# Kernel tuning notes

Measured on AMD Instinct MI355X. Metric: run time of the kernel, lower is better.

Reference implementation:

```python
import jax, jax.numpy as jnp
import numpy as np

LN_EPS = 1e-5


def _layernorm(x, gamma, beta):
    mu = jnp.mean(x, axis=-1, keepdims=True)
    var = jnp.mean(jnp.square(x - mu), axis=-1, keepdims=True)
    return (x - mu) / jnp.sqrt(var + LN_EPS) * gamma + beta


def setup_inputs() -> dict:
    key = jax.random.key(0)
    ks = jax.random.split(key, 4)
    B, T, H, L = 32, 2048, 512, 2
    scale = 1.0 / np.sqrt(H)  # matches torch GRU uniform(-1/sqrt(H),1/sqrt(H)) scale
    x = jax.random.normal(ks[0], (B, T, H), dtype=jnp.float32)
    W_ih = jax.random.normal(ks[1], (L, 3 * H, H), dtype=jnp.float32) * scale
    W_hh = jax.random.normal(ks[2], (L, 3 * H, H), dtype=jnp.float32) * scale
    b_ih = jnp.zeros((L, 3 * H), dtype=jnp.float32)
    b_hh = jnp.zeros((L, 3 * H), dtype=jnp.float32)
    gamma = jnp.ones((H,), dtype=jnp.float32)
    beta = jnp.zeros((H,), dtype=jnp.float32)
    return {"x": x, "gamma": gamma, "beta": beta,
            "W_ih": W_ih, "W_hh": W_hh, "b_ih": b_ih, "b_hh": b_hh}


def reference(x, gamma, beta, W_ih, W_hh, b_ih, b_hh):
    # LayerNorm then multi-layer GRU (PyTorch gate order: r, z, n).
    B, T, H = x.shape
    L = W_ih.shape[0]
    h = _layernorm(x, gamma, beta)
    for l in range(L):
        # Precompute input projections for all timesteps: [B, T, 3H]
        xp = jnp.einsum('bth,gh->btg', h, W_ih[l]) + b_ih[l]
        Whh_l = W_hh[l]
        bhh_l = b_hh[l]

        def step(h_prev, xp_t):
            hp = h_prev @ Whh_l.T + bhh_l              # [B, 3H]
            xr, xz, xn = jnp.split(xp_t, 3, axis=-1)
            hr, hz, hn = jnp.split(hp, 3, axis=-1)
            r = jax.nn.sigmoid(xr + hr)
            z = jax.nn.sigmoid(xz + hz)
            n = jnp.tanh(xn + r * hn)
            h_new = (1.0 - z) * n + z * h_prev
            return h_new, h_new

        h0 = jnp.zeros((B, H), dtype=x.dtype)
        _, ys = jax.lax.scan(step, h0, jnp.swapaxes(xp, 0, 1))  # [T, B, H]
        h = jnp.swapaxes(ys, 0, 1)
    return h
```

## Files before the change

### kernel.cpp

```cpp
#include <hip/hip_runtime.h>
#include <hip/hip_fp16.h>

typedef float f32x4 __attribute__((ext_vector_type(4)));
typedef float f32x16 __attribute__((ext_vector_type(16)));
typedef _Float16 half8 __attribute__((ext_vector_type(8)));
typedef _Float16 half2t __attribute__((ext_vector_type(2)));
typedef unsigned int u32;
typedef u32 u32x4v __attribute__((ext_vector_type(4)));

#define DEVI static __device__ __forceinline__

constexpr int BATCH = 32;
constexpr int TLEN  = 2048;
constexpr int HDIM  = 512;
constexpr int G3    = 1536;

DEVI float fast_sigmoid(float x) { return 1.0f / (1.0f + __expf(-x)); }

DEVI float fast_tanh(float x) {
  const float ax = fabsf(x);
  const float t = __expf(-2.0f * ax);
  const float r = (1.0f - t) / (1.0f + t);
  return copysignf(r, x);
}

DEVI u32 pack2h(float a, float b) {
  return __builtin_bit_cast(u32, __builtin_amdgcn_cvt_pkrtz(a, b));
}

DEVI u32 llc_load32(const u32* p) {
  return __hip_atomic_load(p, __ATOMIC_RELAXED, __HIP_MEMORY_SCOPE_AGENT);
}
DEVI void llc_store32(u32* p, u32 v) {
  __hip_atomic_store(p, v, __ATOMIC_RELAXED, __HIP_MEMORY_SCOPE_AGENT);
}

DEVI u32x4v llc_load128_async(const u32* p) {
  u32x4v r;
  asm volatile("global_load_dwordx4 %0, %1, off sc0 sc1" : "=&v"(r) : "v"(p));
  return r;
}

__global__ void convert_weights(const float* __restrict__ wih, const float* __restrict__ whh,
                                _Float16* __restrict__ wih_h, _Float16* __restrict__ whh_h)
{
  const size_t n = (size_t)2 * G3 * HDIM;
  for (size_t i = (size_t)blockIdx.x * blockDim.x + threadIdx.x; i < n;
       i += (size_t)gridDim.x * blockDim.x) {
    wih_h[i] = (_Float16)wih[i];
    whh_h[i] = (_Float16)whh[i];
  }
}

__global__ __launch_bounds__(256) void ln_kernel(const float* __restrict__ x,
    const float* __restrict__ gamma, const float* __restrict__ beta,
    _Float16* __restrict__ out)
{
  const int row = blockIdx.x;
  const int tid = threadIdx.x;
  const float* xr = x + (size_t)row * HDIM;
  float a = xr[tid], b = xr[tid + 256];
  float s = a + b, ss = a * a + b * b;
#pragma unroll
  for (int m = 1; m < 64; m <<= 1) {
    s  += __shfl_xor(s, m, 64);
    ss += __shfl_xor(ss, m, 64);
  }
  __shared__ float sb[8];
  const int w = tid >> 6;
  if ((tid & 63) == 0) { sb[w] = s; sb[4 + w] = ss; }
  __syncthreads();
  s  = sb[0] + sb[1] + sb[2] + sb[3];
  ss = sb[4] + sb[5] + sb[6] + sb[7];
  const float mu   = s * (1.0f / HDIM);
  const float var  = ss * (1.0f / HDIM) - mu * mu;
  const float rstd = rsqrtf(var + 1e-5f);
  out[(size_t)row * HDIM + tid]       = (_Float16)((a - mu) * rstd * gamma[tid] + beta[tid]);
  out[(size_t)row * HDIM + tid + 256] = (_Float16)((b - mu) * rstd * gamma[tid + 256] + beta[tid + 256]);
}

__global__ __launch_bounds__(256) void gemm_f16(
    const _Float16* __restrict__ A, const _Float16* __restrict__ W,
    const float* __restrict__ bias, _Float16* __restrict__ C,
    int t0, int lgT)
{
  __shared__ _Float16 As[128][40];
  __shared__ _Float16 Bs[128][40];
  const int bm = blockIdx.x;
  const int bn = blockIdx.y;
  const int tid = threadIdx.x;
  const int lane = tid & 63;
  const int wv = tid >> 6;
  const int wm = wv >> 1, wn = wv & 1;
  const int l15 = lane & 15, g4 = lane >> 4;
  const int tmask = (1 << lgT) - 1;

  f32x4 zero4 = {0.f, 0.f, 0.f, 0.f};
  f32x4 acc[4][4];
#pragma unroll
  for (int i = 0; i < 4; ++i) {
#pragma unroll
    for (int j = 0; j < 4; ++j) acc[i][j] = zero4;
  }

  const int srow = tid >> 2;
  const int scol = (tid & 3) * 8;
  size_t arow[2];
#pragma unroll
  for (int r2 = 0; r2 < 2; ++r2) {
    int m = bm * 128 + r2 * 64 + srow;
    int b = m >> lgT, tt = m & tmask;
    arow[r2] = ((size_t)b * TLEN + (size_t)(t0 + tt)) * HDIM;
  }
  const size_t brow0 = (size_t)(bn * 128 + srow) * HDIM;

  for (int kt = 0; kt < HDIM; kt += 32) {
#pragma unroll
    for (int r2 = 0; r2 < 2; ++r2) {
      *(uint4*)&As[r2 * 64 + srow][scol] = *(const uint4*)&A[arow[r2] + kt + scol];
      *(uint4*)&Bs[r2 * 64 + srow][scol] = *(const uint4*)&W[brow0 + (size_t)r2 * 64 * HDIM + kt + scol];
    }
    __syncthreads();
    half8 af[4], bf[4];
#pragma unroll
    for (int i = 0; i < 4; ++i) af[i] = *(const half8*)&As[wm * 64 + i * 16 + l15][g4 * 8];
#pragma unroll
    for (int j = 0; j < 4; ++j) bf[j] = *(const half8*)&Bs[wn * 64 + j * 16 + l15][g4 * 8];
#pragma unroll
    for (int i = 0; i < 4; ++i) {
#pragma unroll
      for (int j = 0; j < 4; ++j)
        acc[i][j] = __builtin_amdgcn_mfma_f32_16x16x32_f16(af[i], bf[j], acc[i][j], 0, 0, 0);
    }
    __syncthreads();
  }
#pragma unroll
  for (int j = 0; j < 4; ++j) {
    const int col = bn * 128 + wn * 64 + j * 16 + l15;
    const float bi = bias[col];
#pragma unroll
    for (int i = 0; i < 4; ++i) {
      const int mrow = bm * 128 + wm * 64 + i * 16 + g4 * 4;
#pragma unroll
      for (int r = 0; r < 4; ++r)
        C[(size_t)(mrow + r) * G3 + col] = (_Float16)(acc[i][j][r] + bi);
    }
  }
}

__global__ void init_sync(u32* __restrict__ hbufs, u32* __restrict__ flags)
{
  const int i = blockIdx.x * 256 + threadIdx.x;
  if (i < 6 * 8192) hbufs[i] = 0u;
  if (i < 64) flags[i] = 0u;
}

__global__ __launch_bounds__(512, 1) void gru_fused(
    const u32* __restrict__ xp,
    const u32* __restrict__ whh,
    const u32* __restrict__ wih2,
    const float* __restrict__ bhh,
    const float* __restrict__ bih2,
    float* __restrict__ out,
    u32* __restrict__ h1buf,
    u32* __restrict__ h2buf,
    u32* __restrict__ flags,
    int t0, int t1, int lgT)
{
  const int l2 = blockIdx.x >> 4;
  const int c  = blockIdx.x & 15;
  const int tid = threadIdx.x;
  const int lane = tid & 63;
  const int w = tid >> 6;
  const int l31 = lane & 31;
  const int kh = lane >> 5;

  __shared__ __align__(16) u32 st_l[32 * 260];
  __shared__ __align__(16) u32 h1_l[32 * 260];
  __shared__ float sg_h[96 * 33];
  __shared__ float sg_i[96 * 33];

  half8 bf[32];
  const bool mfma_w = (w < 3) || (l2 && w < 6);
  if (mfma_w) {
    const int gt = (w < 3) ? w : w - 3;
    const int grow = gt * 512 + c * 32 + l31;
    const u32* wsrc = (w < 3) ? (whh + (size_t)l2 * (G3 * 256)) : wih2;
#pragma unroll
    for (int ks = 0; ks < 32; ++ks)
      bf[ks] = *(const half8*)&wsrc[(size_t)grow * 256 + ks * 8 + kh * 4];
  }

  const int dp = tid & 15;
  const int ga = tid >> 4;
  const float* bhh_l = bhh + l2 * G3;
  float biasH[3][2], biasI[3][2];
#pragma unroll
  for (int gt = 0; gt < 3; ++gt) {
    biasH[gt][0] = bhh_l[gt * 512 + c * 32 + 2 * dp];
    biasH[gt][1] = bhh_l[gt * 512 + c * 32 + 2 * dp + 1];
    biasI[gt][0] = l2 ? bih2[gt * 512 + c * 32 + 2 * dp] : 0.0f;
    biasI[gt][1] = l2 ? bih2[gt * 512 + c * 32 + 2 * dp + 1] : 0.0f;
  }

  for (int t = t0; t < t1; ++t) {
    u32 xu[3];
    if (!l2) {
      const size_t row = ((size_t)(ga << lgT) + (size_t)(t - t0)) * 768;
#pragma unroll
      for (int gt = 0; gt < 3; ++gt)
        xu[gt] = xp[row + gt * 256 + c * 16 + dp];
    }
    if (w == 0) {
      const int n1 = l2 ? (t + 1) : t;
      const int n2 = l2 ? t       : (t - 3);
      const int fl = lane & 15;
      while (true) {
        const int f1 = (int)llc_load32(&flags[fl]);
        const int f2 = (int)llc_load32(&flags[32 + fl]);
        if (__all((int)((f1 >= n1) && (f2 >= n2)))) break;
        __builtin_amdgcn_s_sleep(1);
      }
    }
    __syncthreads();

    const u32* stsrc = l2 ? (h2buf + (size_t)(t & 1) * 8192)
                          : (h1buf + (size_t)(t & 3) * 8192);
    u32x4v sv0, sv1, sv2, sv3, hv0, hv1, hv2, hv3;
    {
      const u32* sp = stsrc + (tid << 2);
      sv0 = llc_load128_async(sp);
      sv1 = llc_load128_async(sp + 2048);
      sv2 = llc_load128_async(sp + 4096);
      sv3 = llc_load128_async(sp + 6144);
      if (l2) {
        const u32* hp = h1buf + (size_t)((t + 1) & 3) * 8192 + (tid << 2);
        hv0 = llc_load128_async(hp);
        hv1 = llc_load128_async(hp + 2048);
        hv2 = llc_load128_async(hp + 4096);
        hv3 = llc_load128_async(hp + 6144);
      }
    }
    asm volatile("s_waitcnt vmcnt(0)" ::: "memory");
    __builtin_amdgcn_sched_barrier(0);
    {
      const int r0 = tid >> 6;
      const int cc = (tid << 2) & 255;
      *(u32x4v*)&st_l[(0  + r0) * 260 + cc] = sv0;
      *(u32x4v*)&st_l[(8  + r0) * 260 + cc] = sv1;
      *(u32x4v*)&st_l[(16 + r0) * 260 + cc] = sv2;
      *(u32x4v*)&st_l[(24 + r0) * 260 + cc] = sv3;
      if (l2) {
        *(u32x4v*)&h1_l[(0  + r0) * 260 + cc] = hv0;
        *(u32x4v*)&h1_l[(8  + r0) * 260 + cc] = hv1;
        *(u32x4v*)&h1_l[(16 + r0) * 260 + cc] = hv2;
        *(u32x4v*)&h1_l[(24 + r0) * 260 + cc] = hv3;
      }
    }
    __syncthreads();

    const u32 hpp = st_l[ga * 260 + c * 16 + dp];

    if (mfma_w) {
      f32x16 acc;
#pragma unroll
      for (int i = 0; i < 16; ++i) acc[i] = 0.0f;
      const u32* asrc = (w < 3) ? st_l : h1_l;
#pragma unroll
      for (int ks = 0; ks < 32; ++ks) {
        const half8 af = *(const half8*)&asrc[l31 * 260 + ks * 8 + kh * 4];
        acc = __builtin_amdgcn_mfma_f32_32x32x16_f16(af, bf[ks], acc, 0, 0, 0);
      }
      const int gt = (w < 3) ? w : w - 3;
      float* sg = (w < 3) ? sg_h : sg_i;
#pragma unroll
      for (int r = 0; r < 16; ++r) {
        const int grp = (r & 3) + 8 * (r >> 2) + 4 * kh;
        sg[(gt * 32 + l31) * 33 + grp] = acc[r];
      }
    }
    __syncthreads();

    float hn0, hn1;
    {
      const half2t hp2 = __builtin_bit_cast(half2t, hpp);
      float hn[2];
#pragma unroll
      for (int dd = 0; dd < 2; ++dd) {
        const int d = 2 * dp + dd;
        float xr, xz, xn;
        if (!l2) {
          const half2t xr2 = __builtin_bit_cast(half2t, xu[0]);
          const half2t xz2 = __builtin_bit_cast(half2t, xu[1]);
          const half2t xn2 = __builtin_bit_cast(half2t, xu[2]);
          xr = (float)(dd ? xr2.y : xr2.x);
          xz = (float)(dd ? xz2.y : xz2.x);
          xn = (float)(dd ? xn2.y : xn2.x);
        } else {
          xr = sg_i[(0 * 32 + d) * 33 + ga] + biasI[0][dd];
          xz = sg_i[(32 + d) * 33 + ga]     + biasI[1][dd];
          xn = sg_i[(64 + d) * 33 + ga]     + biasI[2][dd];
        }
        const float hprev = (float)(dd ? hp2.y : hp2.x);
        const float rr = fast_sigmoid(xr + sg_h[(0 * 32 + d) * 33 + ga] + biasH[0][dd]);
        const float zz = fast_sigmoid(xz + sg_h[(32 + d) * 33 + ga]     + biasH[1][dd]);
        const float nn = fast_tanh(xn + rr * (sg_h[(64 + d) * 33 + ga]  + biasH[2][dd]));
        hn[dd] = (1.0f - zz) * nn + zz * hprev;
      }
      hn0 = hn[0]; hn1 = hn[1];
      if (!l2) {
        llc_store32(&h1buf[(size_t)((t + 1) & 3) * 8192 + ga * 256 + c * 16 + dp],
                    pack2h(hn0, hn1));
      } else {
        llc_store32(&h2buf[(size_t)((t + 1) & 1) * 8192 + ga * 256 + c * 16 + dp],
                    pack2h(hn0, hn1));
      }
    }
    asm volatile("s_waitcnt vmcnt(0)" ::: "memory");
    __syncthreads();
    if (tid == 0)
      llc_store32(&flags[l2 * 32 + c], (u32)(t + 1));
    if (l2) {
      float2 v; v.x = hn0; v.y = hn1;
      *(float2*)&out[((size_t)ga * TLEN + t) * HDIM + c * 32 + 2 * dp] = v;
    }
  }
}

extern "C" void kernel_launch(void* const* d_in, const int* in_sizes, int n_in,
                              void* d_out, int out_size, void* d_ws, size_t ws_size,
                              hipStream_t stream)
{
  const float* x     = (const float*)d_in[0];
  const float* gamma = (const float*)d_in[1];
  const float* beta  = (const float*)d_in[2];
  const float* Wih   = (const float*)d_in[3];
  const float* Whh   = (const float*)d_in[4];
  const float* bih   = (const float*)d_in[5];
  const float* bhh   = (const float*)d_in[6];
  float* out = (float*)d_out;

  const size_t wbytes  = (size_t)2 * G3 * HDIM * 2;
  const size_t hseqb   = (size_t)BATCH * TLEN * HDIM * 2;
  const size_t fixed   = hseqb + 2 * wbytes + (size_t)6 * 8192 * 4 + 64 * 4 + 4096;
  int lgT = 11;
  while (lgT > 2 && ((size_t)BATCH * ((size_t)1 << lgT) * G3 * 2 + fixed) > ws_size) --lgT;
  const int TSEG = 1 << lgT;
  const int nseg = TLEN / TSEG;

  char* ws = (char*)d_ws;
  _Float16* xp    = (_Float16*)ws;
  char* base      = ws + (size_t)BATCH * TSEG * G3 * 2;
  _Float16* hseq  = (_Float16*)base;
  _Float16* wih_h = (_Float16*)(base + hseqb);
  _Float16* whh_h = (_Float16*)(base + hseqb + wbytes);
  u32*      h1buf = (u32*)     (base + hseqb + 2 * wbytes);
  u32*      h2buf = h1buf + (size_t)4 * 8192;
  u32*      flags = h2buf + (size_t)2 * 8192;

  convert_weights<<<512, 256, 0, stream>>>(Wih, Whh, wih_h, whh_h);
  ln_kernel<<<BATCH * TLEN, 256, 0, stream>>>(x, gamma, beta, hseq);
  init_sync<<<192, 256, 0, stream>>>(h1buf, flags);

  const dim3 ggrid(BATCH * TSEG / 128, 12);
  for (int s = 0; s < nseg; ++s) {
    const int t0 = s * TSEG;
    gemm_f16<<<ggrid, 256, 0, stream>>>(hseq, wih_h, bih, xp, t0, lgT);
    gru_fused<<<32, 512, 0, stream>>>((const u32*)xp, (const u32*)whh_h,
                                      (const u32*)(wih_h + (size_t)G3 * HDIM),
                                      bhh, bih + G3, out,
                                      h1buf, h2buf, flags, t0, t0 + TSEG, lgT);
  }
}
```

Before: 9.361 ms.

## Replace flag-based inter-block sync with poison-value ring buffers for hidden states

Replaces the per-block progress flags and barrier-then-load handshake with 16-slot ring buffers whose slots are marked with a poison value. Consumers spin-load the hidden-state data directly and proceed once no poison remains. Producers write the data and re-poison a future slot, with no trailing wait or barrier before signalling. This removes one sync round-trip and a __syncthreads per timestep from the serial recurrence critical path. The cost is larger ring buffers and a correctness dependence on per-word store visibility ordering and on a single layer-2 progress counter for back-pressure.

```diff
diff --git a/kernel.cpp b/kernel.cpp
--- a/kernel.cpp
+++ b/kernel.cpp
@@ -14,6 +14,8 @@
 constexpr int TLEN  = 2048;
 constexpr int HDIM  = 512;
 constexpr int G3    = 1536;
+constexpr u32 POIS  = 0xFFFFFFFFu;
+constexpr int NSLOT = 16;
 
 DEVI float fast_sigmoid(float x) { return 1.0f / (1.0f + __expf(-x)); }
 
@@ -39,6 +41,10 @@
   u32x4v r;
   asm volatile("global_load_dwordx4 %0, %1, off sc0 sc1" : "=&v"(r) : "v"(p));
   return r;
+}
+
+DEVI int chk4(u32x4v v) {
+  return (int)((v[0] == POIS) | (v[1] == POIS) | (v[2] == POIS) | (v[3] == POIS));
 }
 
 __global__ void convert_weights(const float* __restrict__ wih, const float* __restrict__ whh,
@@ -148,11 +154,14 @@
   }
 }
 
-__global__ void init_sync(u32* __restrict__ hbufs, u32* __restrict__ flags)
+__global__ void init_sync(u32* __restrict__ h1ring, u32* __restrict__ h2ring,
+                          u32* __restrict__ syncw)
 {
   const int i = blockIdx.x * 256 + threadIdx.x;
-  if (i < 6 * 8192) hbufs[i] = 0u;
-  if (i < 64) flags[i] = 0u;
+  const u32 v = (i >> 13) == 0 ? 0u : POIS;
+  h1ring[i] = v;
+  h2ring[i] = v;
+  if (i == 0) syncw[0] = 0u;
 }
 
 __global__ __launch_bounds__(512, 1) void gru_fused(
@@ -162,9 +171,9 @@
     const float* __restrict__ bhh,
     const float* __restrict__ bih2,
     float* __restrict__ out,
-    u32* __restrict__ h1buf,
-    u32* __restrict__ h2buf,
-    u32* __restrict__ flags,
+    u32* __restrict__ h1ring,
+    u32* __restrict__ h2ring,
+    u32* __restrict__ syncw,
     int t0, int t1, int lgT)
 {
   const int l2 = blockIdx.x >> 4;
@@ -203,6 +212,8 @@
     biasI[gt][1] = l2 ? bih2[gt * 512 + c * 32 + 2 * dp + 1] : 0.0f;
   }
 
+  u32* const ringOwn = l2 ? h2ring : h1ring;
+
   for (int t = t0; t < t1; ++t) {
     u32 xu[3];
     if (!l2) {
@@ -211,50 +222,43 @@
       for (int gt = 0; gt < 3; ++gt)
         xu[gt] = xp[row + gt * 256 + c * 16 + dp];
     }
-    if (w == 0) {
-      const int n1 = l2 ? (t + 1) : t;
-      const int n2 = l2 ? t       : (t - 3);
-      const int fl = lane & 15;
-      while (true) {
-        const int f1 = (int)llc_load32(&flags[fl]);
-        const int f2 = (int)llc_load32(&flags[32 + fl]);
-        if (__all((int)((f1 >= n1) && (f2 >= n2)))) break;
-        __builtin_amdgcn_s_sleep(1);
-      }
-    }
-    __syncthreads();
-
-    const u32* stsrc = l2 ? (h2buf + (size_t)(t & 1) * 8192)
-                          : (h1buf + (size_t)(t & 3) * 8192);
-    u32x4v sv0, sv1, sv2, sv3, hv0, hv1, hv2, hv3;
-    {
-      const u32* sp = stsrc + (tid << 2);
-      sv0 = llc_load128_async(sp);
-      sv1 = llc_load128_async(sp + 2048);
-      sv2 = llc_load128_async(sp + 4096);
-      sv3 = llc_load128_async(sp + 6144);
+
+    const u32* rdA = ringOwn + (size_t)(t & 15) * 8192 + (tid << 2);
+    const u32* rdB = h1ring + (size_t)((t + 1) & 15) * 8192 + (tid << 2);
+    u32x4v a0, a1, a2, a3, b0, b1, b2, b3;
+    while (true) {
+      a0 = llc_load128_async(rdA);
+      a1 = llc_load128_async(rdA + 2048);
+      a2 = llc_load128_async(rdA + 4096);
+      a3 = llc_load128_async(rdA + 6144);
       if (l2) {
-        const u32* hp = h1buf + (size_t)((t + 1) & 3) * 8192 + (tid << 2);
-        hv0 = llc_load128_async(hp);
-        hv1 = llc_load128_async(hp + 2048);
-        hv2 = llc_load128_async(hp + 4096);
-        hv3 = llc_load128_async(hp + 6144);
-      }
-    }
-    asm volatile("s_waitcnt vmcnt(0)" ::: "memory");
-    __builtin_amdgcn_sched_barrier(0);
+        b0 = llc_load128_async(rdB);
+        b1 = llc_load128_async(rdB + 2048);
+        b2 = llc_load128_async(rdB + 4096);
+        b3 = llc_load128_async(rdB + 6144);
+      }
+      u32 prog = 0;
+      if (!l2) prog = llc_load32(&syncw[0]);
+      asm volatile("s_waitcnt vmcnt(0)" ::: "memory");
+      __builtin_amdgcn_sched_barrier(0);
+      int bad = chk4(a0) | chk4(a1) | chk4(a2) | chk4(a3);
+      if (l2) bad |= chk4(b0) | chk4(b1) | chk4(b2) | chk4(b3);
+      else    bad |= (int)((int)prog < t - 3);
+      if (!__any(bad)) break;
+      __builtin_amdgcn_s_sleep(1);
+    }
     {
       const int r0 = tid >> 6;
       const int cc = (tid << 2) & 255;
-      *(u32x4v*)&st_l[(0  + r0) * 260 + cc] = sv0;
-      *(u32x4v*)&st_l[(8  + r0) * 260 + cc] = sv1;
-      *(u32x4v*)&st_l[(16 + r0) * 260 + cc] = sv2;
-      *(u32x4v*)&st_l[(24 + r0) * 260 + cc] = sv3;
+      *(u32x4v*)&st_l[(0  + r0) * 260 + cc] = a0;
+      *(u32x4v*)&st_l[(8  + r0) * 260 + cc] = a1;
+      *(u32x4v*)&st_l[(16 + r0) * 260 + cc] = a2;
+      *(u32x4v*)&st_l[(24 + r0) * 260 + cc] = a3;
       if (l2) {
-        *(u32x4v*)&h1_l[(0  + r0) * 260 + cc] = hv0;
-        *(u32x4v*)&h1_l[(8  + r0) * 260 + cc] = hv1;
-        *(u32x4v*)&h1_l[(16 + r0) * 260 + cc] = hv2;
-        *(u32x4v*)&h1_l[(24 + r0) * 260 + cc] = hv3;
+        *(u32x4v*)&h1_l[(0  + r0) * 260 + cc] = b0;
+        *(u32x4v*)&h1_l[(8  + r0) * 260 + cc] = b1;
+        *(u32x4v*)&h1_l[(16 + r0) * 260 + cc] = b2;
+        *(u32x4v*)&h1_l[(24 + r0) * 260 + cc] = b3;
       }
     }
     __syncthreads();
@@ -308,22 +312,15 @@
         hn[dd] = (1.0f - zz) * nn + zz * hprev;
       }
       hn0 = hn[0]; hn1 = hn[1];
-      if (!l2) {
-        llc_store32(&h1buf[(size_t)((t + 1) & 3) * 8192 + ga * 256 + c * 16 + dp],
-                    pack2h(hn0, hn1));
-      } else {
-        llc_store32(&h2buf[(size_t)((t + 1) & 1) * 8192 + ga * 256 + c * 16 + dp],
-                    pack2h(hn0, hn1));
-      }
-    }
-    asm volatile("s_waitcnt vmcnt(0)" ::: "memory");
-    __syncthreads();
-    if (tid == 0)
-      llc_store32(&flags[l2 * 32 + c], (u32)(t + 1));
+    }
+    const int my = ga * 256 + c * 16 + dp;
+    llc_store32(&ringOwn[(size_t)((t + 1) & 15) * 8192 + my], pack2h(hn0, hn1));
     if (l2) {
       float2 v; v.x = hn0; v.y = hn1;
       *(float2*)&out[((size_t)ga * TLEN + t) * HDIM + c * 32 + 2 * dp] = v;
     }
+    llc_store32(&ringOwn[(size_t)((t + 9) & 15) * 8192 + my], POIS);
+    if (l2 && c == 0 && tid == 0) llc_store32(&syncw[0], (u32)(t + 1));
   }
 }
 
@@ -342,25 +339,26 @@
 
   const size_t wbytes  = (size_t)2 * G3 * HDIM * 2;
   const size_t hseqb   = (size_t)BATCH * TLEN * HDIM * 2;
-  const size_t fixed   = hseqb + 2 * wbytes + (size_t)6 * 8192 * 4 + 64 * 4 + 4096;
+  const size_t ringb   = (size_t)NSLOT * 8192 * 4;
+  const size_t fixed   = hseqb + 2 * wbytes + 2 * ringb + 4096;
   int lgT = 11;
   while (lgT > 2 && ((size_t)BATCH * ((size_t)1 << lgT) * G3 * 2 + fixed) > ws_size) --lgT;
   const int TSEG = 1 << lgT;
   const int nseg = TLEN / TSEG;
 
   char* ws = (char*)d_ws;
-  _Float16* xp    = (_Float16*)ws;
-  char* base      = ws + (size_t)BATCH * TSEG * G3 * 2;
-  _Float16* hseq  = (_Float16*)base;
-  _Float16* wih_h = (_Float16*)(base + hseqb);
-  _Float16* whh_h = (_Float16*)(base + hseqb + wbytes);
-  u32*      h1buf = (u32*)     (base + hseqb + 2 * wbytes);
-  u32*      h2buf = h1buf + (size_t)4 * 8192;
-  u32*      flags = h2buf + (size_t)2 * 8192;
+  _Float16* xp     = (_Float16*)ws;
+  char* base       = ws + (size_t)BATCH * TSEG * G3 * 2;
+  _Float16* hseq   = (_Float16*)base;
+  _Float16* wih_h  = (_Float16*)(base + hseqb);
+  _Float16* whh_h  = (_Float16*)(base + hseqb + wbytes);
+  u32*      h1ring = (u32*)    (base + hseqb + 2 * wbytes);
+  u32*      h2ring = h1ring + (size_t)NSLOT * 8192;
+  u32*      syncw  = h2ring + (size_t)NSLOT * 8192;
 
   convert_weights<<<512, 256, 0, stream>>>(Wih, Whh, wih_h, whh_h);
   ln_kernel<<<BATCH * TLEN, 256, 0, stream>>>(x, gamma, beta, hseq);
-  init_sync<<<192, 256, 0, stream>>>(h1buf, flags);
+  init_sync<<<512, 256, 0, stream>>>(h1ring, h2ring, syncw);
 
   const dim3 ggrid(BATCH * TSEG / 128, 12);
   for (int s = 0; s < nseg; ++s) {
@@ -369,6 +367,6 @@
     gru_fused<<<32, 512, 0, stream>>>((const u32*)xp, (const u32*)whh_h,
                                       (const u32*)(wih_h + (size_t)G3 * HDIM),
                                       bhh, bih + G3, out,
-                                      h1buf, h2buf, flags, t0, t0 + TSEG, lgT);
-  }
-}
+                                      h1ring, h2ring, syncw, t0, t0 + TSEG, lgT);
+  }
+}
```

Measured after the change: 8.701 ms. -7.0%, faster.
